# Kernel tuning notes

Hardware: AMD Instinct MI355X
Metric: run time of the kernel (lower is better)

## Reference

```python
import jax, jax.numpy as jnp
import numpy as np

B, SQ, QD = 8, 4096, 1280
SCTX, CD = 93, 2048
HEADS, DIM_HEAD = 20, 64
INNER = HEADS * DIM_HEAD  # 1280


def setup_inputs() -> dict:
    key = jax.random.key(0)
    ks = jax.random.split(key, 10)
    inp = {
        'x': jax.random.normal(ks[0], (B, SQ, QD), dtype=jnp.float32),
        'context': jax.random.normal(ks[1], (B, SCTX, CD), dtype=jnp.float32),
        'scale': jax.random.uniform(ks[2], (), dtype=jnp.float32),
        'num_img_token': 16,
        # learned parameters (PyTorch nn.Linear weight layout: [out, in])
        'Wq': jax.random.normal(ks[3], (INNER, QD), dtype=jnp.float32) * 0.02,
        'Wk': jax.random.normal(ks[4], (INNER, CD), dtype=jnp.float32) * 0.02,
        'Wv': jax.random.normal(ks[5], (INNER, CD), dtype=jnp.float32) * 0.02,
        'Wk_ip': jax.random.normal(ks[6], (INNER, CD), dtype=jnp.float32) * 0.02,
        'Wv_ip': jax.random.normal(ks[7], (INNER, CD), dtype=jnp.float32) * 0.02,
        'Wout': jax.random.normal(ks[8], (QD, INNER), dtype=jnp.float32) * 0.02,
        'b_out': jax.random.normal(ks[9], (QD,), dtype=jnp.float32) * 0.02,
    }
    return inp


def _heads(t):
    # [b, s, inner] -> [b, h, s, d]
    b, s, _ = t.shape
    return t.reshape(b, s, HEADS, DIM_HEAD).transpose(0, 2, 1, 3)


def _attn(q, k, v):
    # q: [b,h,sq,d], k/v: [b,h,skv,d]
    sm_scale = 1.0 / jnp.sqrt(jnp.asarray(DIM_HEAD, q.dtype))
    logits = jnp.einsum('bhqd,bhkd->bhqk', q, k) * sm_scale
    probs = jax.nn.softmax(logits, axis=-1)
    return jnp.einsum('bhqk,bhkd->bhqd', probs, v)


def reference(x, context, scale, num_img_token, Wq, Wk, Wv, Wk_ip, Wv_ip, Wout, b_out):
    eos = context.shape[1] - num_img_token
    txt_ctx = context[:, :eos, :]
    img_ctx = context[:, eos:, :]

    q = _heads(jnp.einsum('bsc,ic->bsi', x, Wq))
    k = _heads(jnp.einsum('bsc,ic->bsi', txt_ctx, Wk))
    v = _heads(jnp.einsum('bsc,ic->bsi', txt_ctx, Wv))
    k_i = _heads(jnp.einsum('bsc,ic->bsi', img_ctx, Wk_ip))
    v_i = _heads(jnp.einsum('bsc,ic->bsi', img_ctx, Wv_ip))

    txt_out = _attn(q, k, v)            # [b,h,sq,d]
    img_out = _attn(q, k_i, v_i)        # [b,h,sq,d]
    out = txt_out + scale * img_out

    out = out.transpose(0, 2, 1, 3).reshape(x.shape[0], x.shape[1], INNER)
    return jnp.einsum('bsi,oi->bso', out, Wout) + b_out
```

## Files before the change

### kernel.cpp

```cpp
#include <hip/hip_runtime.h>
#include <stdint.h>
#include <stddef.h>

typedef __attribute__((ext_vector_type(8))) short bf16x8;
typedef __attribute__((ext_vector_type(4))) short bf16x4;
typedef __attribute__((ext_vector_type(4))) float f32x4;

typedef const __attribute__((address_space(1))) uint32_t gas_u32;
typedef __attribute__((address_space(3))) uint32_t las_u32;

__device__ __forceinline__ short f2bf(float f) {
  union { float f; uint32_t u; } c; c.f = f;
  uint32_t u = c.u;
  u += 0x7fffu + ((u >> 16) & 1u);
  return (short)(u >> 16);
}

__global__ void k_cvt(const float* __restrict__ src, short* __restrict__ dst, int n) {
  int i = (blockIdx.x * 256 + threadIdx.x) * 4;
  if (i + 4 <= n) {
    float4 v = *(const float4*)(src + i);
    bf16x4 o = { f2bf(v.x), f2bf(v.y), f2bf(v.z), f2bf(v.w) };
    *(bf16x4*)(dst + i) = o;
  } else {
    for (; i < n; ++i) dst[i] = f2bf(src[i]);
  }
}

__global__ void k_cvt_ctx(const float* __restrict__ ctx, short* __restrict__ dst,
                          int rpb, int row0) {
  long total = 8L * rpb * 2048;
  long i = ((long)blockIdx.x * 256 + threadIdx.x) * 4;
  if (i >= total) return;
  int c = (int)(i & 2047);
  long rs = i >> 11;
  int b = (int)(rs / rpb);
  int s = (int)(rs - (long)b * rpb);
  const float* sp = ctx + ((long)(b * 93 + row0 + s) * 2048 + c);
  float4 v = *(const float4*)sp;
  bf16x4 o = { f2bf(v.x), f2bf(v.y), f2bf(v.z), f2bf(v.w) };
  *(bf16x4*)(dst + i) = o;
}

template <int MODE>
__global__ __launch_bounds__(256)
void k_gemm(const short* __restrict__ A, const short* __restrict__ Bm,
            void* __restrict__ out, const float* __restrict__ bias,
            int Mreal, int N, int K, int SPB) {
  __shared__ __align__(16) short As[128 * 32];
  __shared__ __align__(16) short Bs[128 * 32];
  const int t = threadIdx.x;
  const int lane = t & 63, wave = t >> 6;
  const int wm = (wave >> 1) * 64, wn = (wave & 1) * 64;
  const int m0 = blockIdx.y * 128, n0 = blockIdx.x * 128;
  const int q4 = lane >> 4, r16 = lane & 15;

  f32x4 zero = {0.f, 0.f, 0.f, 0.f};
  f32x4 acc[4][4];
#pragma unroll
  for (int i = 0; i < 4; ++i)
#pragma unroll
    for (int j = 0; j < 4; ++j) acc[i][j] = zero;

  const int c0 = t, c1 = t + 256;
  const int ar0 = c0 >> 2, ao0 = (c0 & 3) * 8;
  const int ar1 = c1 >> 2, ao1 = (c1 & 3) * 8;
  int gm0 = m0 + ar0; if (gm0 >= Mreal) gm0 = Mreal - 1;
  int gm1 = m0 + ar1; if (gm1 >= Mreal) gm1 = Mreal - 1;
  const short* ga0 = A + (size_t)gm0 * K + ao0;
  const short* ga1 = A + (size_t)gm1 * K + ao1;
  const short* gb0 = Bm + (size_t)(n0 + ar0) * K + ao0;
  const short* gb1 = Bm + (size_t)(n0 + ar1) * K + ao1;

  for (int k0 = 0; k0 < K; k0 += 32) {
    __builtin_amdgcn_global_load_lds((gas_u32*)(ga0 + k0), (las_u32*)(As + c0 * 8), 16, 0, 0);
    __builtin_amdgcn_global_load_lds((gas_u32*)(ga1 + k0), (las_u32*)(As + c1 * 8), 16, 0, 0);
    __builtin_amdgcn_global_load_lds((gas_u32*)(gb0 + k0), (las_u32*)(Bs + c0 * 8), 16, 0, 0);
    __builtin_amdgcn_global_load_lds((gas_u32*)(gb1 + k0), (las_u32*)(Bs + c1 * 8), 16, 0, 0);
    __syncthreads();

    bf16x8 af[4], bf[4];
#pragma unroll
    for (int i = 0; i < 4; ++i)
      af[i] = *(const bf16x8*)(As + (wm + i * 16 + r16) * 32 + q4 * 8);
#pragma unroll
    for (int j = 0; j < 4; ++j)
      bf[j] = *(const bf16x8*)(Bs + (wn + j * 16 + r16) * 32 + q4 * 8);
#pragma unroll
    for (int i = 0; i < 4; ++i)
#pragma unroll
      for (int j = 0; j < 4; ++j)
        acc[i][j] = __builtin_amdgcn_mfma_f32_16x16x32_bf16(af[i], bf[j], acc[i][j], 0, 0, 0);
    __syncthreads();
  }

  if (MODE == 0) {
    short* O = (short*)out;
#pragma unroll
    for (int i = 0; i < 4; ++i) {
#pragma unroll
      for (int rr = 0; rr < 4; ++rr) {
        int m = m0 + wm + i * 16 + q4 * 4 + rr;
        if (m < Mreal) {
          int bb, ss;
          if (SPB == 4096) { bb = m >> 12; ss = m & 4095; }
          else             { bb = m / SPB; ss = m - bb * SPB; }
#pragma unroll
          for (int j = 0; j < 4; ++j) {
            int n = n0 + wn + j * 16 + r16;
            int h = n >> 6, d = n & 63;
            O[(((size_t)(bb * 20 + h)) * SPB + ss) * 64 + d] = f2bf(acc[i][j][rr]);
          }
        }
      }
    }
  } else {
    float* O = (float*)out;
#pragma unroll
    for (int i = 0; i < 4; ++i) {
#pragma unroll
      for (int rr = 0; rr < 4; ++rr) {
        int m = m0 + wm + i * 16 + q4 * 4 + rr;
        if (m < Mreal) {
#pragma unroll
          for (int j = 0; j < 4; ++j) {
            int n = n0 + wn + j * 16 + r16;
            O[(size_t)m * N + n] = acc[i][j][rr] + bias[n];
          }
        }
      }
    }
  }
}

__global__ __launch_bounds__(256)
void k_attn(const short* __restrict__ qb, const short* __restrict__ kb,
            const short* __restrict__ vb, const short* __restrict__ kib,
            const short* __restrict__ vib, const float* __restrict__ scale_p,
            short* __restrict__ out) {
  constexpr int KS = 72;
  constexpr int PS = 104;
  __shared__ __align__(16) short Ks[96 * KS];
  __shared__ __align__(16) short Vt[64 * PS];
  __shared__ __align__(16) short Pp[4][16 * PS];
  const int t = threadIdx.x, lane = t & 63, wave = t >> 6;
  const int q4 = lane >> 4, r16 = lane & 15;
  const int b = blockIdx.z, h = blockIdx.y, qt = blockIdx.x;
  const int bh = b * 20 + h;
  const short* kt = kb + (size_t)bh * 77 * 64;
  const short* vt = vb + (size_t)bh * 77 * 64;
  const short* ki = kib + (size_t)bh * 16 * 64;
  const short* vi = vib + (size_t)bh * 16 * 64;

  for (int c = t; c < 96 * 8; c += 256) {
    int row = c >> 3, o = (c & 7) * 8;
    uint4 val = {0u, 0u, 0u, 0u};
    if (row < 77)       val = *(const uint4*)(kt + row * 64 + o);
    else if (row >= 80) val = *(const uint4*)(ki + (row - 80) * 64 + o);
    *(uint4*)(Ks + row * KS + o) = val;
  }
  for (int i = t; i < 96 * 64; i += 256) {
    int key = i >> 6, d = i & 63;
    short v = 0;
    if (key < 77)       v = vt[key * 64 + d];
    else if (key >= 80) v = vi[(key - 80) * 64 + d];
    Vt[d * PS + key] = v;
  }
  __syncthreads();

  const int s0 = qt * 64 + wave * 16;
  const short* qp = qb + ((size_t)bh * 4096 + s0) * 64;
  bf16x8 qf[2];
#pragma unroll
  for (int kc = 0; kc < 2; ++kc)
    qf[kc] = *(const bf16x8*)(qp + r16 * 64 + kc * 32 + q4 * 8);

  f32x4 zero = {0.f, 0.f, 0.f, 0.f};
  f32x4 lg[6];
#pragma unroll
  for (int nt = 0; nt < 6; ++nt) {
    lg[nt] = zero;
#pragma unroll
    for (int kc = 0; kc < 2; ++kc) {
      bf16x8 kf = *(const bf16x8*)(Ks + (nt * 16 + r16) * KS + kc * 32 + q4 * 8);
      lg[nt] = __builtin_amdgcn_mfma_f32_16x16x32_bf16(qf[kc], kf, lg[nt], 0, 0, 0);
    }
  }

  const float sm = 0.125f;
  const float scl = scale_p[0];
#pragma unroll
  for (int nt = 0; nt < 6; ++nt)
#pragma unroll
    for (int rr = 0; rr < 4; ++rr) lg[nt][rr] *= sm;
  if (r16 >= 13) {
#pragma unroll
    for (int rr = 0; rr < 4; ++rr) lg[4][rr] = -1e30f;
  }

#pragma unroll
  for (int rr = 0; rr < 4; ++rr) {
    float mx = -1e30f;
#pragma unroll
    for (int nt = 0; nt < 5; ++nt) mx = fmaxf(mx, lg[nt][rr]);
#pragma unroll
    for (int o = 1; o < 16; o <<= 1) mx = fmaxf(mx, __shfl_xor(mx, o, 64));
    float s = 0.f;
#pragma unroll
    for (int nt = 0; nt < 5; ++nt) {
      float p = __expf(lg[nt][rr] - mx);
      lg[nt][rr] = p; s += p;
    }
#pragma unroll
    for (int o = 1; o < 16; o <<= 1) s += __shfl_xor(s, o, 64);
    float inv = 1.f / s;
#pragma unroll
    for (int nt = 0; nt < 5; ++nt) lg[nt][rr] *= inv;

    float mi = lg[5][rr];
#pragma unroll
    for (int o = 1; o < 16; o <<= 1) mi = fmaxf(mi, __shfl_xor(mi, o, 64));
    float pi = __expf(lg[5][rr] - mi);
    float si = pi;
#pragma unroll
    for (int o = 1; o < 16; o <<= 1) si += __shfl_xor(si, o, 64);
    lg[5][rr] = pi * (scl / si);
  }

  short* pw = &Pp[wave][0];
#pragma unroll
  for (int nt = 0; nt < 6; ++nt)
#pragma unroll
    for (int rr = 0; rr < 4; ++rr)
      pw[(q4 * 4 + rr) * PS + nt * 16 + r16] = f2bf(lg[nt][rr]);

  f32x4 oc[4];
#pragma unroll
  for (int dt = 0; dt < 4; ++dt) {
    oc[dt] = zero;
#pragma unroll
    for (int kc = 0; kc < 3; ++kc) {
      bf16x8 pf = *(const bf16x8*)(pw + r16 * PS + kc * 32 + q4 * 8);
      bf16x8 vf = *(const bf16x8*)(Vt + (dt * 16 + r16) * PS + kc * 32 + q4 * 8);
      oc[dt] = __builtin_amdgcn_mfma_f32_16x16x32_bf16(pf, vf, oc[dt], 0, 0, 0);
    }
  }

#pragma unroll
  for (int dt = 0; dt < 4; ++dt)
#pragma unroll
    for (int rr = 0; rr < 4; ++rr) {
      int m = s0 + q4 * 4 + rr;
      int d = dt * 16 + r16;
      out[((size_t)b * 4096 + m) * 1280 + h * 64 + d] = f2bf(oc[dt][rr]);
    }
}

extern "C" void kernel_launch(void* const* d_in, const int* in_sizes, int n_in,
                              void* d_out, int out_size, void* d_ws, size_t ws_size,
                              hipStream_t stream) {
  const float* x    = (const float*)d_in[0];
  const float* ctx  = (const float*)d_in[1];
  const float* scal = (const float*)d_in[2];
  const float* Wq   = (const float*)d_in[4];
  const float* Wk   = (const float*)d_in[5];
  const float* Wv   = (const float*)d_in[6];
  const float* Wkip = (const float*)d_in[7];
  const float* Wvip = (const float*)d_in[8];
  const float* Wout = (const float*)d_in[9];
  const float* bout = (const float*)d_in[10];
  float* out = (float*)d_out;

  char* ws = (char*)d_ws;
  size_t off = 0;
  auto alloc = [&](size_t elems) -> short* {
    short* p = (short*)(ws + off);
    off += (elems * 2 + 255) & ~(size_t)255;
    return p;
  };
  short* xb    = alloc(32768UL * 1280);
  short* txtb  = alloc(616UL * 2048);
  short* imgb  = alloc(128UL * 2048);
  short* Wqb   = alloc(1280UL * 1280);
  short* Wkb   = alloc(1280UL * 2048);
  short* Wvb   = alloc(1280UL * 2048);
  short* Wkipb = alloc(1280UL * 2048);
  short* Wvipb = alloc(1280UL * 2048);
  short* Woutb = alloc(1280UL * 1280);
  short* qb    = alloc(32768UL * 1280);
  short* kb    = alloc(160UL * 77 * 64);
  short* vb    = alloc(160UL * 77 * 64);
  short* kib   = alloc(160UL * 16 * 64);
  short* vib   = alloc(160UL * 16 * 64);
  short* attnb = xb;

  auto cvt = [&](const float* s, short* d, long n) {
    int blocks = (int)((n / 4 + 255) / 256);
    k_cvt<<<blocks, 256, 0, stream>>>(s, d, (int)n);
  };
  cvt(x, xb, 32768L * 1280);
  cvt(Wq, Wqb, 1280L * 1280);
  cvt(Wk, Wkb, 1280L * 2048);
  cvt(Wv, Wvb, 1280L * 2048);
  cvt(Wkip, Wkipb, 1280L * 2048);
  cvt(Wvip, Wvipb, 1280L * 2048);
  cvt(Wout, Woutb, 1280L * 1280);
  {
    long n1 = 8L * 77 * 2048;
    k_cvt_ctx<<<(int)((n1 / 4 + 255) / 256), 256, 0, stream>>>(ctx, txtb, 77, 0);
    long n2 = 8L * 16 * 2048;
    k_cvt_ctx<<<(int)((n2 / 4 + 255) / 256), 256, 0, stream>>>(ctx, imgb, 16, 77);
  }

  { dim3 g(10, 256); k_gemm<0><<<g, 256, 0, stream>>>(xb, Wqb, qb, nullptr, 32768, 1280, 1280, 4096); }
  { dim3 g(10, 5);
    k_gemm<0><<<g, 256, 0, stream>>>(txtb, Wkb, kb, nullptr, 616, 1280, 2048, 77);
    k_gemm<0><<<g, 256, 0, stream>>>(txtb, Wvb, vb, nullptr, 616, 1280, 2048, 77); }
  { dim3 g(10, 1);
    k_gemm<0><<<g, 256, 0, stream>>>(imgb, Wkipb, kib, nullptr, 128, 1280, 2048, 16);
    k_gemm<0><<<g, 256, 0, stream>>>(imgb, Wvipb, vib, nullptr, 128, 1280, 2048, 16); }
  { dim3 g(64, 20, 8);
    k_attn<<<g, 256, 0, stream>>>(qb, kb, vb, kib, vib, scal, attnb); }
  { dim3 g(10, 256);
    k_gemm<1><<<g, 256, 0, stream>>>(attnb, Woutb, out, bout, 32768, 1280, 1280, 1); }
}
```

Baseline: 976.6 us.

## Swizzle GEMM LDS tiles and merge K/V projections into single GEMMs

Applies an XOR swizzle to the 16-byte column chunks of the LDS tiles. The global source address is permuted so each chunk lands at a swizzled position, and MFMA fragment reads use the matching swizzle, which is meant to cut LDS bank conflicts. Separately, the K and V weights (and the image K/V weights) are packed into one concatenated matrix. Each pair is then computed with one GEMM of width 2560 instead of two launches, and the epilogue routes heads at or above 20 into the second (V) buffer. This removes launches and doubles the small-GEMM grid width, but adds index arithmetic to the epilogue.

```diff
diff --git a/kernel.cpp b/kernel.cpp
--- a/kernel.cpp
+++ b/kernel.cpp
@@ -62,30 +62,32 @@
 #pragma unroll
     for (int j = 0; j < 4; ++j) acc[i][j] = zero;
 
-  const int c0 = t, c1 = t + 256;
-  const int ar0 = c0 >> 2, ao0 = (c0 & 3) * 8;
-  const int ar1 = c1 >> 2, ao1 = (c1 & 3) * 8;
+  const int p0 = t, p1 = t + 256;
+  const int ar0 = p0 >> 2, ac0 = (((p0 & 3) ^ ((ar0 >> 1) & 3))) * 8;
+  const int ar1 = p1 >> 2, ac1 = (((p1 & 3) ^ ((ar1 >> 1) & 3))) * 8;
   int gm0 = m0 + ar0; if (gm0 >= Mreal) gm0 = Mreal - 1;
   int gm1 = m0 + ar1; if (gm1 >= Mreal) gm1 = Mreal - 1;
-  const short* ga0 = A + (size_t)gm0 * K + ao0;
-  const short* ga1 = A + (size_t)gm1 * K + ao1;
-  const short* gb0 = Bm + (size_t)(n0 + ar0) * K + ao0;
-  const short* gb1 = Bm + (size_t)(n0 + ar1) * K + ao1;
+  const short* ga0 = A + (size_t)gm0 * K + ac0;
+  const short* ga1 = A + (size_t)gm1 * K + ac1;
+  const short* gb0 = Bm + (size_t)(n0 + ar0) * K + ac0;
+  const short* gb1 = Bm + (size_t)(n0 + ar1) * K + ac1;
+
+  const int swz = (q4 ^ ((r16 >> 1) & 3)) * 8;
 
   for (int k0 = 0; k0 < K; k0 += 32) {
-    __builtin_amdgcn_global_load_lds((gas_u32*)(ga0 + k0), (las_u32*)(As + c0 * 8), 16, 0, 0);
-    __builtin_amdgcn_global_load_lds((gas_u32*)(ga1 + k0), (las_u32*)(As + c1 * 8), 16, 0, 0);
-    __builtin_amdgcn_global_load_lds((gas_u32*)(gb0 + k0), (las_u32*)(Bs + c0 * 8), 16, 0, 0);
-    __builtin_amdgcn_global_load_lds((gas_u32*)(gb1 + k0), (las_u32*)(Bs + c1 * 8), 16, 0, 0);
+    __builtin_amdgcn_global_load_lds((gas_u32*)(ga0 + k0), (las_u32*)(As + p0 * 8), 16, 0, 0);
+    __builtin_amdgcn_global_load_lds((gas_u32*)(ga1 + k0), (las_u32*)(As + p1 * 8), 16, 0, 0);
+    __builtin_amdgcn_global_load_lds((gas_u32*)(gb0 + k0), (las_u32*)(Bs + p0 * 8), 16, 0, 0);
+    __builtin_amdgcn_global_load_lds((gas_u32*)(gb1 + k0), (las_u32*)(Bs + p1 * 8), 16, 0, 0);
     __syncthreads();
 
     bf16x8 af[4], bf[4];
 #pragma unroll
     for (int i = 0; i < 4; ++i)
-      af[i] = *(const bf16x8*)(As + (wm + i * 16 + r16) * 32 + q4 * 8);
+      af[i] = *(const bf16x8*)(As + (wm + i * 16 + r16) * 32 + swz);
 #pragma unroll
     for (int j = 0; j < 4; ++j)
-      bf[j] = *(const bf16x8*)(Bs + (wn + j * 16 + r16) * 32 + q4 * 8);
+      bf[j] = *(const bf16x8*)(Bs + (wn + j * 16 + r16) * 32 + swz);
 #pragma unroll
     for (int i = 0; i < 4; ++i)
 #pragma unroll
@@ -109,7 +111,9 @@
           for (int j = 0; j < 4; ++j) {
             int n = n0 + wn + j * 16 + r16;
             int h = n >> 6, d = n & 63;
-            O[(((size_t)(bb * 20 + h)) * SPB + ss) * 64 + d] = f2bf(acc[i][j][rr]);
+            int grp = (h >= 20) ? 1 : 0;
+            int hl = h - grp * 20;
+            O[(((size_t)(grp * 160 + bb * 20 + hl)) * SPB + ss) * 64 + d] = f2bf(acc[i][j][rr]);
           }
         }
       }
@@ -282,16 +286,14 @@
   short* txtb  = alloc(616UL * 2048);
   short* imgb  = alloc(128UL * 2048);
   short* Wqb   = alloc(1280UL * 1280);
-  short* Wkb   = alloc(1280UL * 2048);
-  short* Wvb   = alloc(1280UL * 2048);
-  short* Wkipb = alloc(1280UL * 2048);
-  short* Wvipb = alloc(1280UL * 2048);
+  short* Wkvb  = alloc(2UL * 1280 * 2048);
+  short* Wkvip = alloc(2UL * 1280 * 2048);
   short* Woutb = alloc(1280UL * 1280);
   short* qb    = alloc(32768UL * 1280);
-  short* kb    = alloc(160UL * 77 * 64);
-  short* vb    = alloc(160UL * 77 * 64);
-  short* kib   = alloc(160UL * 16 * 64);
-  short* vib   = alloc(160UL * 16 * 64);
+  short* kb    = alloc(2UL * 160 * 77 * 64);
+  short* kib   = alloc(2UL * 160 * 16 * 64);
+  short* vb    = kb  + 160UL * 77 * 64;
+  short* vib   = kib + 160UL * 16 * 64;
   short* attnb = xb;
 
   auto cvt = [&](const float* s, short* d, long n) {
@@ -300,10 +302,10 @@
   };
   cvt(x, xb, 32768L * 1280);
   cvt(Wq, Wqb, 1280L * 1280);
-  cvt(Wk, Wkb, 1280L * 2048);
-  cvt(Wv, Wvb, 1280L * 2048);
-  cvt(Wkip, Wkipb, 1280L * 2048);
-  cvt(Wvip, Wvipb, 1280L * 2048);
+  cvt(Wk,   Wkvb,                 1280L * 2048);
+  cvt(Wv,   Wkvb + 1280L * 2048,  1280L * 2048);
+  cvt(Wkip, Wkvip,                1280L * 2048);
+  cvt(Wvip, Wkvip + 1280L * 2048, 1280L * 2048);
   cvt(Wout, Woutb, 1280L * 1280);
   {
     long n1 = 8L * 77 * 2048;
@@ -313,12 +315,10 @@
   }
 
   { dim3 g(10, 256); k_gemm<0><<<g, 256, 0, stream>>>(xb, Wqb, qb, nullptr, 32768, 1280, 1280, 4096); }
-  { dim3 g(10, 5);
-    k_gemm<0><<<g, 256, 0, stream>>>(txtb, Wkb, kb, nullptr, 616, 1280, 2048, 77);
-    k_gemm<0><<<g, 256, 0, stream>>>(txtb, Wvb, vb, nullptr, 616, 1280, 2048, 77); }
-  { dim3 g(10, 1);
-    k_gemm<0><<<g, 256, 0, stream>>>(imgb, Wkipb, kib, nullptr, 128, 1280, 2048, 16);
-    k_gemm<0><<<g, 256, 0, stream>>>(imgb, Wvipb, vib, nullptr, 128, 1280, 2048, 16); }
+  { dim3 g(20, 5);
+    k_gemm<0><<<g, 256, 0, stream>>>(txtb, Wkvb, kb, nullptr, 616, 2560, 2048, 77); }
+  { dim3 g(20, 1);
+    k_gemm<0><<<g, 256, 0, stream>>>(imgb, Wkvip, kib, nullptr, 128, 2560, 2048, 16); }
   { dim3 g(64, 20, 8);
     k_attn<<<g, 256, 0, stream>>>(qb, kb, vb, kib, vib, scal, attnb); }
   { dim3 g(10, 256);
```

New measurement: 882.8 us. 1.11x faster.
